# Kernel optimization log

Measured on AMD Instinct MI355X. Metric: run time of the kernel, lower is better.

## Reference

```python
import jax, jax.numpy as jnp
import numpy as np

BN_EPS = 1e-5


def setup_inputs() -> dict:
    key = jax.random.key(0)
    ks = jax.random.split(key, 8)
    B, C, T, H, W = 8, 64, 16, 56, 56
    Cr = C // 4  # ratio=4 bottleneck in RouteFuncMLP
    s = lambda k, shape, scale=0.05: jax.random.normal(k, shape, jnp.float32) * scale
    return {
        "x": jax.random.normal(ks[0], (B, C, T, H, W), jnp.float32),
        "view": 3,  # View.FOUL
        "emb": s(ks[1], (4, C), 1.0),
        "Wg": s(ks[2], (C, C)),
        "bg": jnp.zeros((C,), jnp.float32),
        "Wa": s(ks[3], (Cr, C, 3)),
        "ba": jnp.zeros((Cr,), jnp.float32),
        "bn_gamma": jnp.ones((Cr,), jnp.float32),
        "bn_beta": jnp.zeros((Cr,), jnp.float32),
        "bn_mean": jnp.zeros((Cr,), jnp.float32),
        "bn_var": jnp.ones((Cr,), jnp.float32),
        "Wb": s(ks[4], (C, Cr, 3)),
        "Wconv": s(ks[5], (C, C, 3, 3)),
        "Wcls": s(ks[6], (10, C)),
        "bcls": jnp.zeros((10,), jnp.float32),
    }


def _conv1d_t(x, w, pad):
    # Temporal conv: x [B, Cin, T], w [Cout, Cin, K] -> [B, Cout, T]
    return jax.lax.conv_general_dilated(
        x, w, window_strides=(1,), padding=[(pad, pad)],
        dimension_numbers=("NCH", "OIH", "NCH"))


def _route_func(x, Wg, bg, Wa, ba, bn_gamma, bn_beta, bn_mean, bn_var, Wb):
    # RouteFuncMLP: per-frame, per-channel calibration factors. x: [B,C,T,H,W]
    g = x.mean(axis=(2, 3, 4))  # global pool -> [B,C]
    xt = x.mean(axis=(3, 4))    # spatial pool -> [B,C,T]
    g = jnp.einsum("oc,bc->bo", Wg, g) + bg  # 1x1x1 conv on global branch
    h = _conv1d_t(xt + g[:, :, None], Wa, pad=1) + ba[None, :, None]  # [B,Cr,T]
    # BatchNorm3d (inference form with running stats)
    h = (h - bn_mean[None, :, None]) * jax.lax.rsqrt(bn_var[None, :, None] + BN_EPS)
    h = h * bn_gamma[None, :, None] + bn_beta[None, :, None]
    h = jax.nn.relu(h)
    return _conv1d_t(h, Wb, pad=1) + 1.0  # alpha: [B,C,T]


def reference(x, view, emb, Wg, bg, Wa, ba, bn_gamma, bn_beta, bn_mean, bn_var, Wb, Wconv, Wcls, bcls):
    B, C, T, H, W = x.shape
    # embed-add: broadcast the view embedding over T,H,W
    x = x + emb[view][None, :, None, None, None]
    alpha = _route_func(x, Wg, bg, Wa, ba, bn_gamma, bn_beta, bn_mean, bn_var, Wb)
    # TAdaConv2d with cal_dim='cin': scaling the shared kernel per input channel
    # (per batch, per frame) is mathematically identical to scaling the input
    # channels first and convolving with the shared kernel.
    xs = x * alpha[:, :, :, None, None]
    xs = xs.transpose(0, 2, 1, 3, 4).reshape(B * T, C, H, W)
    y = jax.lax.conv_general_dilated(
        xs, Wconv, window_strides=(1, 1), padding=[(1, 1), (1, 1)],
        dimension_numbers=("NCHW", "OIHW", "NCHW"))
    y = y.reshape(B, T, C, H, W).transpose(0, 2, 1, 3, 4)  # [B,C,T,H,W]
    pooled = y.max(axis=(2, 3, 4))  # max over T,H,W -> [B,C]
    return pooled @ Wcls.T + bcls   # [B,10]
```

## Files before the change

kernel.cpp:

```cpp
#include <hip/hip_runtime.h>
#include <math.h>

#define B_ 8
#define C_ 64
#define T_ 16
#define H_ 56
#define W_ 56
#define HW_ (H_ * W_)
#define CR_ 16
#define PLANE (T_ * HW_)

typedef __attribute__((ext_vector_type(8))) short bf16x8;
typedef __attribute__((ext_vector_type(4))) float f32x4;

__device__ __forceinline__ unsigned short f2bf(float f) {
    unsigned u = __float_as_uint(f);
    u += 0x7fffu + ((u >> 16) & 1u);
    return (unsigned short)(u >> 16);
}

__device__ __forceinline__ void gload_lds16(const void* g, void* l) {
    __builtin_amdgcn_global_load_lds(
        (const __attribute__((address_space(1))) unsigned int*)g,
        (__attribute__((address_space(3))) unsigned int*)l,
        16, 0, 0);
}

__global__ __launch_bounds__(128) void pool_prepack_kernel(
    const float* __restrict__ x, const float* __restrict__ Wconv,
    float* __restrict__ xt, unsigned short* __restrict__ packWbf)
{
    int blk = blockIdx.x;
    int tid = threadIdx.x;
    if (blk >= 8192) {
        int idx = (blk - 8192) * 128 + tid;
        if (idx < 64 * 576) {
            int j     = idx & 7;
            int lane  = (idx >> 3) & 63;
            int mt    = (idx >> 9) & 3;
            int kstep = idx >> 11;
            int cih = kstep & 1, tap = kstep >> 1;
            int co = mt * 16 + (lane & 15);
            int ci = cih * 32 + (lane >> 4) * 8 + j;
            packWbf[idx] = f2bf(Wconv[(co * C_ + ci) * 9 + tap]);
        }
        return;
    }
    __shared__ float red[2];
    const float4* p = (const float4*)(x + (size_t)blk * HW_);
    float s = 0.f;
    #pragma unroll
    for (int k = 0; k < 7; ++k) {
        int i = tid + k * 128;
        if (i < 784) { float4 v = p[i]; s += (v.x + v.y) + (v.z + v.w); }
    }
    #pragma unroll
    for (int off = 32; off > 0; off >>= 1) s += __shfl_down(s, off);
    if ((tid & 63) == 0) red[tid >> 6] = s;
    __syncthreads();
    if (tid == 0) xt[blk] = red[0] + red[1];
}

#define LCOLS2 58
#define HROWE (4 * LCOLS2)

__global__ __launch_bounds__(256) void conv_mfma_kernel(
    const float* __restrict__ x, const float* __restrict__ emb,
    const int* __restrict__ viewp, const float* __restrict__ xt,
    const float* __restrict__ Wg, const float* __restrict__ bg,
    const float* __restrict__ Wa, const float* __restrict__ ba,
    const float* __restrict__ bng, const float* __restrict__ bnb,
    const float* __restrict__ bnm, const float* __restrict__ bnv,
    const float* __restrict__ Wb,
    const unsigned short* __restrict__ packWbf, float* __restrict__ part)
{
    __shared__ bf16x8 ltile[10 * HROWE];
    __shared__ float fbuf[8 * 560];
    __shared__ float sa[C_], sea[C_];
    __shared__ float smax[4][C_];

    int blk = blockIdx.x;
    int strip = blk % 7;
    int bt = blk / 7;
    int b = bt >> 4, t = bt & 15;
    int h0 = strip * 8;
    int tid = threadIdx.x;
    int lane = tid & 63, wv = tid >> 6;
    int q4 = lane >> 4, li = lane & 15;

    float* scr = (float*)ltile;
    float* z   = scr;
    float* swa = scr + 1152;
    float* hsv = scr + 4288;
    float* ggv = scr + 4352;
    float* gsv = scr + 4416;

    {
        int view = viewp[0];
        for (int i = tid; i < 1024; i += 256) {
            int c = i >> 4, tt = i & 15;
            z[c * 18 + tt + 1] = xt[b * 1024 + i] * (1.f / HW_) + emb[view * C_ + c];
        }
        if (tid < 128) { int c = tid & 63; z[c * 18 + (tid < 64 ? 0 : 17)] = 0.f; }
        for (int i = tid; i < 3072; i += 256) {
            float v = Wa[i];
            int r = i / 192, rem = i - r * 192;
            int ii = rem / 3, tap = rem - ii * 3;
            swa[ii * 49 + r * 3 + tap] = v;
        }
    }
    __syncthreads();
    if (tid < 64) {
        float s = 0.f;
        #pragma unroll
        for (int k = 1; k <= 16; ++k) s += z[tid * 18 + k];
        gsv[tid] = s * (1.f / 16.f);
    }
    __syncthreads();
    {
        float p = 0.f;
        const float* wrow = Wg + tid * 16;
        int q = tid & 3;
        #pragma unroll
        for (int k = 0; k < 16; ++k) p = fmaf(wrow[k], gsv[q * 16 + k], p);
        p += __shfl_xor(p, 1);
        p += __shfl_xor(p, 2);
        if (q == 0) ggv[tid >> 2] = p + bg[tid >> 2];
    }
    __syncthreads();
    for (int i = tid; i < 1024; i += 256) {
        int c = i >> 4, tt = i & 15;
        z[c * 18 + tt + 1] += ggv[c];
    }
    __syncthreads();
    if (tid < 48) {
        int r = tid & 15, s = tid >> 4;
        int tp = t - 1 + s;
        float hv = 0.f;
        if ((unsigned)tp < 16u) {
            float v = ba[r];
            #pragma unroll 8
            for (int i2 = 0; i2 < 64; ++i2) {
                const float* wa = swa + i2 * 49 + r * 3;
                const float* zr = z + i2 * 18 + tp;
                v = fmaf(zr[0], wa[0], v);
                v = fmaf(zr[1], wa[1], v);
                v = fmaf(zr[2], wa[2], v);
            }
            v = (v - bnm[r]) * rsqrtf(bnv[r] + 1e-5f);
            v = fmaf(v, bng[r], bnb[r]);
            hv = fmaxf(v, 0.f);
        }
        hsv[r * 3 + s] = hv;
    }
    __syncthreads();
    {
        float p = 0.f;
        const float* wrow = Wb + tid * 12;
        int q = tid & 3;
        #pragma unroll
        for (int k = 0; k < 12; ++k) p = fmaf(wrow[k], hsv[q * 12 + k], p);
        p += __shfl_xor(p, 1);
        p += __shfl_xor(p, 2);
        if (q == 0) {
            int c = tid >> 2;
            float a = p + 1.f;
            sa[c] = a;
            sea[c] = emb[viewp[0] * C_ + c] * a;
        }
    }
    __syncthreads();

    if (tid >= 64 && tid < 144) {
        int i = tid - 64;
        int r = i / 8, c8 = i - r * 8;
        int ch4 = c8 >> 1, col = (c8 & 1) ? 57 : 0;
        ltile[(r * 4 + ch4) * LCOLS2 + col] = (bf16x8){0,0,0,0,0,0,0,0};
    }

    const float* xb = x + ((size_t)(b * C_) * T_ + t) * HW_;

    int row0   = (h0 == 0) ? 0 : h0 - 1;
    int rend   = (h0 + 9 > 56) ? 56 : h0 + 9;
    int bytes  = (rend - row0) * 224;
    int ldsoff = (h0 == 0) ? 56 : 0;

    int baddr[7];
    #pragma unroll
    for (int nt = 0; nt < 7; ++nt) {
        int p = (wv * 7 + nt) * 16 + li;
        int row = p / W_, col = p - row * W_;
        baddr[nt] = row * HROWE + q4 * LCOLS2 + col;
    }

    f32x4 acc[7][4];
    #pragma unroll
    for (int nt = 0; nt < 7; ++nt)
        #pragma unroll
        for (int mt = 0; mt < 4; ++mt)
            acc[nt][mt] = (f32x4){0.f, 0.f, 0.f, 0.f};

    const bf16x8* pw = (const bf16x8*)packWbf;

    #pragma unroll
    for (int half = 0; half < 2; ++half) {
        for (int g = 0; g < 4; ++g) {
            #pragma unroll
            for (int pj = 0; pj < 2; ++pj) {
                int j = wv * 2 + pj;
                const char* src = (const char*)(xb +
                    (size_t)(half * 32 + g * 8 + j) * PLANE + row0 * W_);
                float* dst = fbuf + j * 560 + ldsoff;
                #pragma unroll
                for (int s = 0; s < 3; ++s) {
                    if (lane * 16 + s * 1024 < bytes)
                        gload_lds16(src + s * 1024 + lane * 16, dst + s * 256);
                }
            }
            __syncthreads();
            if (tid < 140) {
                int row = tid / 14, cq = tid - row * 14;
                bool valid = !((h0 == 0 && row == 0) || (h0 == 48 && row == 9));
                int ci0 = half * 32 + g * 8;
                bf16x8 hv[4] = {(bf16x8){0,0,0,0,0,0,0,0}, (bf16x8){0,0,0,0,0,0,0,0},
                                (bf16x8){0,0,0,0,0,0,0,0}, (bf16x8){0,0,0,0,0,0,0,0}};
                if (valid) {
                    float4 f[8];
                    #pragma unroll
                    for (int j = 0; j < 8; ++j)
                        f[j] = *(const float4*)&fbuf[j * 560 + row * 56 + cq * 4];
                    #pragma unroll
                    for (int j = 0; j < 8; ++j) {
                        float aj = sa[ci0 + j], ej = sea[ci0 + j];
                        hv[0][j] = (short)f2bf(fmaf(f[j].x, aj, ej));
                        hv[1][j] = (short)f2bf(fmaf(f[j].y, aj, ej));
                        hv[2][j] = (short)f2bf(fmaf(f[j].z, aj, ej));
                        hv[3][j] = (short)f2bf(fmaf(f[j].w, aj, ej));
                    }
                }
                bf16x8* dst = &ltile[(row * 4 + g) * LCOLS2 + cq * 4 + 1];
                #pragma unroll
                for (int cc = 0; cc < 4; ++cc) dst[cc] = hv[cc];
            }
            __syncthreads();
        }

        #pragma unroll
        for (int tap = 0; tap < 9; ++tap) {
            const int kh = tap / 3, kw = tap % 3;
            const int kstep = tap * 2 + half;
            const int boff = kh * HROWE + kw;
            bf16x8 af[4];
            #pragma unroll
            for (int mt = 0; mt < 4; ++mt)
                af[mt] = pw[(kstep * 4 + mt) * 64 + lane];
            #pragma unroll
            for (int nt = 0; nt < 7; ++nt) {
                bf16x8 bfr = ltile[baddr[nt] + boff];
                #pragma unroll
                for (int mt = 0; mt < 4; ++mt)
                    acc[nt][mt] = __builtin_amdgcn_mfma_f32_16x16x32_bf16(
                        af[mt], bfr, acc[nt][mt], 0, 0, 0);
            }
        }
        if (half == 0) __syncthreads();
    }

    float m[4][4];
    #pragma unroll
    for (int mt = 0; mt < 4; ++mt)
        #pragma unroll
        for (int i = 0; i < 4; ++i) {
            float v = acc[0][mt][i];
            #pragma unroll
            for (int nt = 1; nt < 7; ++nt) v = fmaxf(v, acc[nt][mt][i]);
            m[mt][i] = v;
        }
    #pragma unroll
    for (int off = 1; off < 16; off <<= 1)
        #pragma unroll
        for (int mt = 0; mt < 4; ++mt)
            #pragma unroll
            for (int i = 0; i < 4; ++i)
                m[mt][i] = fmaxf(m[mt][i], __shfl_xor(m[mt][i], off));
    if (li == 0) {
        #pragma unroll
        for (int mt = 0; mt < 4; ++mt)
            #pragma unroll
            for (int i = 0; i < 4; ++i)
                smax[wv][mt * 16 + q4 * 4 + i] = m[mt][i];
    }
    __syncthreads();
    if (tid < C_) {
        float mm = fmaxf(fmaxf(smax[0][tid], smax[1][tid]),
                         fmaxf(smax[2][tid], smax[3][tid]));
        part[(size_t)blk * C_ + tid] = mm;
    }
}

__global__ __launch_bounds__(512) void cls_kernel(
    const float* __restrict__ part, const float* __restrict__ Wcls,
    const float* __restrict__ bcls, float* __restrict__ out)
{
    __shared__ float pooled[512];
    int tid = threadIdx.x;
    int b = tid >> 6, c = tid & 63;
    const float* pb = part + (size_t)b * 112 * C_ + c;
    float m0 = -INFINITY, m1 = -INFINITY, m2 = -INFINITY, m3 = -INFINITY;
    #pragma unroll
    for (int i = 0; i < 28; ++i) {
        m0 = fmaxf(m0, pb[(i     ) * C_]);
        m1 = fmaxf(m1, pb[(i + 28) * C_]);
        m2 = fmaxf(m2, pb[(i + 56) * C_]);
        m3 = fmaxf(m3, pb[(i + 84) * C_]);
    }
    pooled[tid] = fmaxf(fmaxf(m0, m1), fmaxf(m2, m3));
    __syncthreads();
    if (tid < B_ * 10) {
        int bb = tid / 10, k = tid - (tid / 10) * 10;
        float v = bcls[k];
        #pragma unroll 8
        for (int cc = 0; cc < C_; ++cc)
            v = fmaf(pooled[bb * C_ + cc], Wcls[k * C_ + cc], v);
        out[tid] = v;
    }
}

extern "C" void kernel_launch(void* const* d_in, const int* in_sizes, int n_in,
                              void* d_out, int out_size, void* d_ws, size_t ws_size,
                              hipStream_t stream)
{
    const float* x     = (const float*)d_in[0];
    const int*   view  = (const int*)  d_in[1];
    const float* emb   = (const float*)d_in[2];
    const float* Wg    = (const float*)d_in[3];
    const float* bg    = (const float*)d_in[4];
    const float* Wa    = (const float*)d_in[5];
    const float* ba    = (const float*)d_in[6];
    const float* bng   = (const float*)d_in[7];
    const float* bnb   = (const float*)d_in[8];
    const float* bnm   = (const float*)d_in[9];
    const float* bnv   = (const float*)d_in[10];
    const float* Wb    = (const float*)d_in[11];
    const float* Wconv = (const float*)d_in[12];
    const float* Wcls  = (const float*)d_in[13];
    const float* bcls  = (const float*)d_in[14];
    float* out = (float*)d_out;

    char* wsb = (char*)d_ws;
    float*          xt      = (float*)(wsb + 0);
    float*          part    = (float*)(wsb + 32768);
    unsigned short* packWbf = (unsigned short*)(wsb + 262144);

    hipLaunchKernelGGL(pool_prepack_kernel, dim3(8192 + 288), dim3(128), 0, stream,
                       x, Wconv, xt, packWbf);
    hipLaunchKernelGGL(conv_mfma_kernel, dim3(B_ * T_ * 7), dim3(256), 0, stream,
                       x, emb, view, xt, Wg, bg, Wa, ba, bng, bnb, bnm, bnv, Wb,
                       packWbf, part);
    hipLaunchKernelGGL(cls_kernel, dim3(1), dim3(512), 0, stream,
                       part, Wcls, bcls, out);
}
```

Before: 84.97 us.

## Double-buffer input channel-group loads and prefetch them before route computation

Input slabs for each 8-channel group are now loaded into two alternating LDS buffers, and the first two groups are issued at kernel start so they overlap the route-function MLP prologue. The loop waits on vmcnt counters rather than full barriers after each issue, and always loads a fixed 10-row window, clamped and shifted by a row offset, so the boundary-dependent byte counts go away. Barriers become explicit lgkmcnt waits so outstanding global-to-LDS loads are not drained early. This adds LDS usage for the second buffer, which may lower occupancy, and it depends on the hand-counted vmcnt values being correct.

```diff
diff --git a/kernel.cpp b/kernel.cpp
--- a/kernel.cpp
+++ b/kernel.cpp
@@ -25,6 +25,12 @@
         (__attribute__((address_space(3))) unsigned int*)l,
         16, 0, 0);
 }
+
+#define BAR_LGKM() do { \
+    asm volatile("s_waitcnt lgkmcnt(0)" ::: "memory"); \
+    __builtin_amdgcn_sched_barrier(0); \
+    __builtin_amdgcn_s_barrier(); \
+    __builtin_amdgcn_sched_barrier(0); } while (0)
 
 __global__ __launch_bounds__(128) void pool_prepack_kernel(
     const float* __restrict__ x, const float* __restrict__ Wconv,
@@ -64,6 +70,22 @@
 #define LCOLS2 58
 #define HROWE (4 * LCOLS2)
 
+__device__ __forceinline__ void issue_grp(const float* xb, float* dstbuf,
+                                          int g, int row0, int wv, int lane)
+{
+    #pragma unroll
+    for (int pj = 0; pj < 2; ++pj) {
+        int j = wv * 2 + pj;
+        const char* src = (const char*)(xb + (size_t)(g * 8 + j) * PLANE
+                                        + (size_t)row0 * W_);
+        float* dst = dstbuf + j * 560;
+        gload_lds16(src + lane * 16, dst);
+        gload_lds16(src + 1024 + lane * 16, dst + 256);
+        if (lane < 12)
+            gload_lds16(src + 2048 + lane * 16, dst + 512);
+    }
+}
+
 __global__ __launch_bounds__(256) void conv_mfma_kernel(
     const float* __restrict__ x, const float* __restrict__ emb,
     const int* __restrict__ viewp, const float* __restrict__ xt,
@@ -75,7 +97,7 @@
     const unsigned short* __restrict__ packWbf, float* __restrict__ part)
 {
     __shared__ bf16x8 ltile[10 * HROWE];
-    __shared__ float fbuf[8 * 560];
+    __shared__ float fbuf[2][8 * 560];
     __shared__ float sa[C_], sea[C_];
     __shared__ float smax[4][C_];
 
@@ -88,6 +110,14 @@
     int lane = tid & 63, wv = tid >> 6;
     int q4 = lane >> 4, li = lane & 15;
 
+    int row0 = h0 - 1; if (row0 < 0) row0 = 0; if (row0 > 46) row0 = 46;
+    int d    = (h0 == 0) ? -1 : ((h0 == 48) ? 1 : 0);
+
+    const float* xb = x + ((size_t)(b * C_) * T_ + t) * HW_;
+
+    issue_grp(xb, fbuf[0], 0, row0, wv, lane);
+    issue_grp(xb, fbuf[1], 1, row0, wv, lane);
+
     float* scr = (float*)ltile;
     float* z   = scr;
     float* swa = scr + 1152;
@@ -109,14 +139,14 @@
             swa[ii * 49 + r * 3 + tap] = v;
         }
     }
-    __syncthreads();
+    BAR_LGKM();
     if (tid < 64) {
         float s = 0.f;
         #pragma unroll
         for (int k = 1; k <= 16; ++k) s += z[tid * 18 + k];
         gsv[tid] = s * (1.f / 16.f);
     }
-    __syncthreads();
+    BAR_LGKM();
     {
         float p = 0.f;
         const float* wrow = Wg + tid * 16;
@@ -127,12 +157,12 @@
         p += __shfl_xor(p, 2);
         if (q == 0) ggv[tid >> 2] = p + bg[tid >> 2];
     }
-    __syncthreads();
+    BAR_LGKM();
     for (int i = tid; i < 1024; i += 256) {
         int c = i >> 4, tt = i & 15;
         z[c * 18 + tt + 1] += ggv[c];
     }
-    __syncthreads();
+    BAR_LGKM();
     if (tid < 48) {
         int r = tid & 15, s = tid >> 4;
         int tp = t - 1 + s;
@@ -153,7 +183,7 @@
         }
         hsv[r * 3 + s] = hv;
     }
-    __syncthreads();
+    BAR_LGKM();
     {
         float p = 0.f;
         const float* wrow = Wb + tid * 12;
@@ -169,7 +199,7 @@
             sea[c] = emb[viewp[0] * C_ + c] * a;
         }
     }
-    __syncthreads();
+    BAR_LGKM();
 
     if (tid >= 64 && tid < 144) {
         int i = tid - 64;
@@ -178,13 +208,6 @@
         ltile[(r * 4 + ch4) * LCOLS2 + col] = (bf16x8){0,0,0,0,0,0,0,0};
     }
 
-    const float* xb = x + ((size_t)(b * C_) * T_ + t) * HW_;
-
-    int row0   = (h0 == 0) ? 0 : h0 - 1;
-    int rend   = (h0 + 9 > 56) ? 56 : h0 + 9;
-    int bytes  = (rend - row0) * 224;
-    int ldsoff = (h0 == 0) ? 56 : 0;
-
     int baddr[7];
     #pragma unroll
     for (int nt = 0; nt < 7; ++nt) {
@@ -203,32 +226,28 @@
     const bf16x8* pw = (const bf16x8*)packWbf;
 
     #pragma unroll
-    for (int half = 0; half < 2; ++half) {
-        for (int g = 0; g < 4; ++g) {
-            #pragma unroll
-            for (int pj = 0; pj < 2; ++pj) {
-                int j = wv * 2 + pj;
-                const char* src = (const char*)(xb +
-                    (size_t)(half * 32 + g * 8 + j) * PLANE + row0 * W_);
-                float* dst = fbuf + j * 560 + ldsoff;
-                #pragma unroll
-                for (int s = 0; s < 3; ++s) {
-                    if (lane * 16 + s * 1024 < bytes)
-                        gload_lds16(src + s * 1024 + lane * 16, dst + s * 256);
-                }
-            }
-            __syncthreads();
+    for (int g = 0; g < 8; ++g) {
+        if (g < 7) { asm volatile("s_waitcnt vmcnt(6)" ::: "memory"); }
+        else       { asm volatile("s_waitcnt vmcnt(0)" ::: "memory"); }
+        __builtin_amdgcn_sched_barrier(0);
+        __builtin_amdgcn_s_barrier();
+        __builtin_amdgcn_sched_barrier(0);
+
+        {
+            const int half = g >> 2, ch4 = g & 3;
+            const float* fb = fbuf[g & 1];
             if (tid < 140) {
                 int row = tid / 14, cq = tid - row * 14;
                 bool valid = !((h0 == 0 && row == 0) || (h0 == 48 && row == 9));
-                int ci0 = half * 32 + g * 8;
+                int ci0 = half * 32 + ch4 * 8;
                 bf16x8 hv[4] = {(bf16x8){0,0,0,0,0,0,0,0}, (bf16x8){0,0,0,0,0,0,0,0},
                                 (bf16x8){0,0,0,0,0,0,0,0}, (bf16x8){0,0,0,0,0,0,0,0}};
                 if (valid) {
+                    int fr = row + d;
                     float4 f[8];
                     #pragma unroll
                     for (int j = 0; j < 8; ++j)
-                        f[j] = *(const float4*)&fbuf[j * 560 + row * 56 + cq * 4];
+                        f[j] = *(const float4*)&fb[j * 560 + fr * 56 + cq * 4];
                     #pragma unroll
                     for (int j = 0; j < 8; ++j) {
                         float aj = sa[ci0 + j], ej = sea[ci0 + j];
@@ -238,32 +257,36 @@
                         hv[3][j] = (short)f2bf(fmaf(f[j].w, aj, ej));
                     }
                 }
-                bf16x8* dst = &ltile[(row * 4 + g) * LCOLS2 + cq * 4 + 1];
+                bf16x8* dst = &ltile[(row * 4 + ch4) * LCOLS2 + cq * 4 + 1];
                 #pragma unroll
                 for (int cc = 0; cc < 4; ++cc) dst[cc] = hv[cc];
             }
-            __syncthreads();
-        }
-
-        #pragma unroll
-        for (int tap = 0; tap < 9; ++tap) {
-            const int kh = tap / 3, kw = tap % 3;
-            const int kstep = tap * 2 + half;
-            const int boff = kh * HROWE + kw;
-            bf16x8 af[4];
+        }
+        BAR_LGKM();
+
+        if (g + 2 <= 7) issue_grp(xb, fbuf[g & 1], g + 2, row0, wv, lane);
+
+        if ((g & 3) == 3) {
+            const int half = g >> 2;
             #pragma unroll
-            for (int mt = 0; mt < 4; ++mt)
-                af[mt] = pw[(kstep * 4 + mt) * 64 + lane];
-            #pragma unroll
-            for (int nt = 0; nt < 7; ++nt) {
-                bf16x8 bfr = ltile[baddr[nt] + boff];
+            for (int tap = 0; tap < 9; ++tap) {
+                const int kh = tap / 3, kw = tap % 3;
+                const int kstep = tap * 2 + half;
+                const int boff = kh * HROWE + kw;
+                bf16x8 af[4];
                 #pragma unroll
                 for (int mt = 0; mt < 4; ++mt)
-                    acc[nt][mt] = __builtin_amdgcn_mfma_f32_16x16x32_bf16(
-                        af[mt], bfr, acc[nt][mt], 0, 0, 0);
+                    af[mt] = pw[(kstep * 4 + mt) * 64 + lane];
+                #pragma unroll
+                for (int nt = 0; nt < 7; ++nt) {
+                    bf16x8 bfr = ltile[baddr[nt] + boff];
+                    #pragma unroll
+                    for (int mt = 0; mt < 4; ++mt)
+                        acc[nt][mt] = __builtin_amdgcn_mfma_f32_16x16x32_bf16(
+                            af[mt], bfr, acc[nt][mt], 0, 0, 0);
+                }
             }
         }
-        if (half == 0) __syncthreads();
     }
 
     float m[4][4];
```

Result: slower. 126.8 us (+49.3%).
